# Kernel tuning notes

Measured on AMD Instinct MI355X. Metric: run time of the kernel, lower is better.

The kernel has to match this reference:

```python
import jax, jax.numpy as jnp
import numpy as np

NEG = -1e9  # masked_fill value


def _forward(input1, input2, wg1, wg2):
    S, E = input1.shape[0], wg1.shape[0]
    k = E // 4                      # expert_group_size
    num_2nd = E // 4
    capacity = int(2 * ((S + num_2nd - 1) // num_2nd))  # training-mode capacity, cf=1.0

    # --- first-level group gating ---
    group_logits = input1 @ wg1.T                     # [S,E]
    group_gates = jax.nn.softmax(group_logits.at[:, 0].set(NEG), axis=1)
    _, top_idx = jax.lax.top_k(group_gates, k)        # [S,k]
    rows = jnp.arange(S)[:, None]
    group_mask = jnp.zeros((S, E), dtype=bool).at[rows, top_idx].set(True)

    # --- second-level logits, masked to the selected group ---
    logits = input2 @ wg2.T                           # [S,E]
    gates = jax.nn.softmax(jnp.where(group_mask, logits, NEG), axis=1)

    # --- htop1gating ---
    indices1 = jnp.argmax(gates, axis=1)              # [S]
    mask1 = jax.nn.one_hot(indices1, E, dtype=jnp.int32)   # [S,E]
    gates1_s = (gates * mask1).sum(axis=1)            # [S]
    locations1 = jnp.cumsum(mask1, axis=0) - 1        # [S,E]

    me = jnp.mean(gates, axis=0)
    ce = jnp.mean(mask1.astype(gates.dtype), axis=0)
    l_aux = jnp.sum(me * ce) / num_2nd * (E * E)

    mask1 = mask1 * (locations1 < capacity).astype(mask1.dtype)
    locations1_s = jnp.sum(locations1 * mask1, axis=1)          # [S]
    gates1 = gates1_s[:, None] * mask1.astype(gates1_s.dtype)   # [S,E]
    locations1_sc = jax.nn.one_hot(locations1_s, capacity, dtype=gates1.dtype)  # [S,C]
    combine = gates1[:, :, None] * locations1_sc[:, None, :]    # [S,E,C]
    dispatch = combine.astype(bool)
    return l_aux, combine, dispatch


def setup_inputs() -> dict:
    key = jax.random.key(0)
    k1, k2, k3, k4 = jax.random.split(key, 4)
    S, D, E = 4096, 1024, 64
    return {
        "input1": jax.random.normal(k1, (S, D), dtype=jnp.float32),
        "input2": jax.random.normal(k2, (S, D), dtype=jnp.float32),
        "wg1": jax.random.normal(k3, (E, D), dtype=jnp.float32) * 0.02,
        "wg2": jax.random.normal(k4, (E, D), dtype=jnp.float32) * 0.02,
    }


def reference(input1, input2, wg1, wg2):
    return _forward(input1, input2, wg1, wg2)
```

## Files before the change

### kernel.cpp

```cpp
#include <hip/hip_runtime.h>
#include <cstdint>
#include <cstddef>

#define S_ROWS 4096
#define DIM 1024
#define NE 64
#define CAP 512
#define NEGV -1e9f

typedef float v4f __attribute__((ext_vector_type(4)));

__global__ __launch_bounds__(256) void zerofill(v4f* __restrict__ out4, long long n4,
                                                float* __restrict__ out, long long n) {
    long long i = (long long)blockIdx.x * blockDim.x + threadIdx.x;
    long long stride = (long long)gridDim.x * blockDim.x;
    v4f z = {0.f, 0.f, 0.f, 0.f};
    for (; i < n4; i += stride) __builtin_nontemporal_store(z, &out4[i]);
    if (blockIdx.x == 0 && threadIdx.x == 0) {
        for (long long j = n4 * 4; j < n; ++j) out[j] = 0.f;
    }
}

__global__ __launch_bounds__(256) void gemm64(const float* __restrict__ X1, const float* __restrict__ W1,
                                              const float* __restrict__ X2, const float* __restrict__ W2,
                                              float* __restrict__ L1, float* __restrict__ L2,
                                              float* __restrict__ Gg, int* __restrict__ Cg) {
    if (blockIdx.x == 0 && blockIdx.y == 0 && threadIdx.x < NE) {
        Gg[threadIdx.x] = 0.f;
        Cg[threadIdx.x] = 0;
    }
    const float* __restrict__ X = blockIdx.y ? X2 : X1;
    const float* __restrict__ W = blockIdx.y ? W2 : W1;
    float* __restrict__ L = blockIdx.y ? L2 : L1;

    __shared__ float As[32][68];
    __shared__ float Bs[64][68];

    const int tid = threadIdx.x;
    const int row0 = blockIdx.x * 32;
    const int tx = tid & 15;
    const int ty = tid >> 4;

    float acc[2][4] = {};

    for (int kk = 0; kk < DIM; kk += 64) {
        __syncthreads();
        #pragma unroll
        for (int p = 0; p < 2; ++p) {
            int r  = (tid >> 4) + p * 16;
            int c4 = (tid & 15) * 4;
            float4 a = *(const float4*)&X[(size_t)(row0 + r) * DIM + kk + c4];
            *(float4*)&As[r][c4] = a;
        }
        #pragma unroll
        for (int p = 0; p < 4; ++p) {
            int e  = (tid >> 4) + p * 16;
            int c4 = (tid & 15) * 4;
            float4 w = *(const float4*)&W[(size_t)e * DIM + kk + c4];
            Bs[c4 + 0][e] = w.x;
            Bs[c4 + 1][e] = w.y;
            Bs[c4 + 2][e] = w.z;
            Bs[c4 + 3][e] = w.w;
        }
        __syncthreads();
        #pragma unroll
        for (int k4 = 0; k4 < 64; k4 += 4) {
            float4 a[2], b[4];
            #pragma unroll
            for (int i = 0; i < 2; ++i) a[i] = *(float4*)&As[ty * 2 + i][k4];
            #pragma unroll
            for (int t = 0; t < 4; ++t) b[t] = *(float4*)&Bs[k4 + t][tx * 4];
            #pragma unroll
            for (int i = 0; i < 2; ++i) {
                acc[i][0] += a[i].x * b[0].x + a[i].y * b[1].x + a[i].z * b[2].x + a[i].w * b[3].x;
                acc[i][1] += a[i].x * b[0].y + a[i].y * b[1].y + a[i].z * b[2].y + a[i].w * b[3].y;
                acc[i][2] += a[i].x * b[0].z + a[i].y * b[1].z + a[i].z * b[2].z + a[i].w * b[3].z;
                acc[i][3] += a[i].x * b[0].w + a[i].y * b[1].w + a[i].z * b[2].w + a[i].w * b[3].w;
            }
        }
    }
    #pragma unroll
    for (int i = 0; i < 2; ++i) {
        float4 v; v.x = acc[i][0]; v.y = acc[i][1]; v.z = acc[i][2]; v.w = acc[i][3];
        *(float4*)&L[(size_t)(row0 + ty * 2 + i) * NE + tx * 4] = v;
    }
}

__global__ __launch_bounds__(256) void gatek2(const float* __restrict__ L1, const float* __restrict__ L2,
                                              int* __restrict__ eidx, float* __restrict__ gval,
                                              float* __restrict__ Gg, int* __restrict__ Cg) {
    __shared__ float sG[4][NE];
    __shared__ int hist[NE];
    const int wid = threadIdx.x >> 6, lane = threadIdx.x & 63;
    if (threadIdx.x < NE) hist[threadIdx.x] = 0;
    __syncthreads();

    const int r0 = blockIdx.x * 16 + wid * 4;
    float gacc = 0.f;
    #pragma unroll
    for (int i = 0; i < 4; ++i) {
        const int r = r0 + i;
        float l1 = L1[(size_t)r * NE + lane];
        if (lane == 0) l1 = NEGV;

        int cnt = 0;
        #pragma unroll
        for (int j = 0; j < 64; ++j) {
            float vj = __shfl(l1, j);
            cnt += (vj > l1 || (vj == l1 && j < lane));
        }
        const bool sel = cnt < 16;

        float l2 = L2[(size_t)r * NE + lane];
        float ml = sel ? l2 : NEGV;

        float m = ml;
        #pragma unroll
        for (int o = 32; o; o >>= 1) m = fmaxf(m, __shfl_xor(m, o));
        float ex = expf(ml - m);
        float sum = ex;
        #pragma unroll
        for (int o = 32; o; o >>= 1) sum += __shfl_xor(sum, o);
        float g = ex / sum;
        gacc += g;

        float bg = g; int bi = lane;
        #pragma unroll
        for (int o = 32; o; o >>= 1) {
            float og = __shfl_xor(bg, o);
            int   oi = __shfl_xor(bi, o);
            if (og > bg || (og == bg && oi < bi)) { bg = og; bi = oi; }
        }
        if (lane == 0) {
            eidx[r] = bi;
            gval[r] = bg;
            atomicAdd(&hist[bi], 1);
        }
    }
    sG[wid][lane] = gacc;
    __syncthreads();
    if (threadIdx.x < NE) {
        float g4 = sG[0][threadIdx.x] + sG[1][threadIdx.x] + sG[2][threadIdx.x] + sG[3][threadIdx.x];
        atomicAdd(&Gg[threadIdx.x], g4);
        atomicAdd(&Cg[threadIdx.x], hist[threadIdx.x]);
    }
}

__global__ void lauxfin(const float* __restrict__ Gg, const int* __restrict__ Cg,
                        float* __restrict__ out) {
    const int lane = threadIdx.x;
    float v = Gg[lane] * (float)Cg[lane];
    #pragma unroll
    for (int o = 32; o; o >>= 1) v += __shfl_xor(v, o);
    if (lane == 0) out[0] = v * (1.0f / 65536.0f);
}

__global__ __launch_bounds__(256) void scatterk(const int* __restrict__ eidx, const float* __restrict__ gval,
                                                float* __restrict__ out) {
    const int s = blockIdx.x;
    const int my = eidx[s];
    int cnt = 0;
    for (int j = threadIdx.x; j < s; j += 256) cnt += (eidx[j] == my);
    __shared__ int sc[4];
    #pragma unroll
    for (int o = 32; o; o >>= 1) cnt += __shfl_down(cnt, o);
    const int wid = threadIdx.x >> 6, lane = threadIdx.x & 63;
    if (lane == 0) sc[wid] = cnt;
    __syncthreads();
    if (threadIdx.x == 0) {
        int rank = sc[0] + sc[1] + sc[2] + sc[3];
        if (rank < CAP) {
            size_t base = 1 + (((size_t)s * NE + my) * CAP + (size_t)rank);
            out[base] = gval[s];
            out[base + (size_t)S_ROWS * NE * CAP] = 1.0f;
        }
    }
}

extern "C" void kernel_launch(void* const* d_in, const int* in_sizes, int n_in,
                              void* d_out, int out_size, void* d_ws, size_t ws_size,
                              hipStream_t stream) {
    const float* in1 = (const float*)d_in[0];
    const float* in2 = (const float*)d_in[1];
    const float* wg1 = (const float*)d_in[2];
    const float* wg2 = (const float*)d_in[3];
    float* out = (float*)d_out;

    float* L1   = (float*)d_ws;
    float* L2   = L1 + (size_t)S_ROWS * NE;
    int*   eidx = (int*)(L2 + (size_t)S_ROWS * NE);
    float* gv   = (float*)(eidx + S_ROWS);
    float* Gg   = gv + S_ROWS;
    int*   Cg   = (int*)(Gg + NE);

    long long n  = (long long)out_size;
    long long n4 = n >> 2;
    zerofill<<<4096, 256, 0, stream>>>((v4f*)out, n4, out, n);

    dim3 g(128, 2);
    gemm64<<<g, 256, 0, stream>>>(in1, wg1, in2, wg2, L1, L2, Gg, Cg);
    gatek2<<<S_ROWS / 16, 256, 0, stream>>>(L1, L2, eidx, gv, Gg, Cg);
    lauxfin<<<1, 64, 0, stream>>>(Gg, Cg, out);
    scatterk<<<S_ROWS, 256, 0, stream>>>(eidx, gv, out);
}
```

Before: 1.185 ms.

## Fuse zero-fill, both gate GEMMs and gating into one launch

Merges the output zero-fill, the two logit GEMMs and the gating step into one kernel. Extra blocks do the fill while the first 128 blocks compute both GEMMs into shared memory and gate directly from there. Global atomics for the aux loss are replaced by per-block slots, which a final kernel reduces together with the scatter. This removes launch gaps and the round trip of logits through global memory, and lets the gating compute overlap the bandwidth-bound fill. In exchange, the GEMM now runs on half as many blocks.

Result: faster. 1.075 ms (-9.2%).

```diff
diff --git a/kernel.cpp b/kernel.cpp
--- a/kernel.cpp
+++ b/kernel.cpp
@@ -7,100 +7,98 @@
 #define NE 64
 #define CAP 512
 #define NEGV -1e9f
+#define NGEMM 128
+#define NFILL 4096
 
 typedef float v4f __attribute__((ext_vector_type(4)));
 
-__global__ __launch_bounds__(256) void zerofill(v4f* __restrict__ out4, long long n4,
-                                                float* __restrict__ out, long long n) {
-    long long i = (long long)blockIdx.x * blockDim.x + threadIdx.x;
-    long long stride = (long long)gridDim.x * blockDim.x;
-    v4f z = {0.f, 0.f, 0.f, 0.f};
-    for (; i < n4; i += stride) __builtin_nontemporal_store(z, &out4[i]);
-    if (blockIdx.x == 0 && threadIdx.x == 0) {
-        for (long long j = n4 * 4; j < n; ++j) out[j] = 0.f;
-    }
-}
-
-__global__ __launch_bounds__(256) void gemm64(const float* __restrict__ X1, const float* __restrict__ W1,
+__global__ __launch_bounds__(256) void fusedA(const float* __restrict__ X1, const float* __restrict__ W1,
                                               const float* __restrict__ X2, const float* __restrict__ W2,
-                                              float* __restrict__ L1, float* __restrict__ L2,
-                                              float* __restrict__ Gg, int* __restrict__ Cg) {
-    if (blockIdx.x == 0 && blockIdx.y == 0 && threadIdx.x < NE) {
-        Gg[threadIdx.x] = 0.f;
-        Cg[threadIdx.x] = 0;
-    }
-    const float* __restrict__ X = blockIdx.y ? X2 : X1;
-    const float* __restrict__ W = blockIdx.y ? W2 : W1;
-    float* __restrict__ L = blockIdx.y ? L2 : L1;
+                                              int* __restrict__ eidx, float* __restrict__ gval,
+                                              float* __restrict__ Gslot, int* __restrict__ Cslot,
+                                              v4f* __restrict__ out4, long long n4,
+                                              float* __restrict__ out, long long n) {
+    const int bid = blockIdx.x;
+    const int tid = threadIdx.x;
 
     __shared__ float As[32][68];
     __shared__ float Bs[64][68];
-
-    const int tid = threadIdx.x;
-    const int row0 = blockIdx.x * 32;
+    __shared__ float Lg[2][32][68];
+    __shared__ float sG[4][NE];
+    __shared__ int   hist[NE];
+
+    if (bid >= NGEMM) {
+        long long i = (long long)(bid - NGEMM) * 256 + tid;
+        const long long stride = (long long)(gridDim.x - NGEMM) * 256;
+        v4f z = {0.f, 0.f, 0.f, 0.f};
+        for (; i < n4; i += stride) __builtin_nontemporal_store(z, &out4[i]);
+        if (bid == NGEMM && tid == 0)
+            for (long long j = n4 * 4; j < n; ++j) out[j] = 0.f;
+        return;
+    }
+
+    if (tid < NE) hist[tid] = 0;
+
+    const int row0 = bid * 32;
     const int tx = tid & 15;
     const int ty = tid >> 4;
 
-    float acc[2][4] = {};
-
-    for (int kk = 0; kk < DIM; kk += 64) {
-        __syncthreads();
-        #pragma unroll
-        for (int p = 0; p < 2; ++p) {
-            int r  = (tid >> 4) + p * 16;
-            int c4 = (tid & 15) * 4;
-            float4 a = *(const float4*)&X[(size_t)(row0 + r) * DIM + kk + c4];
-            *(float4*)&As[r][c4] = a;
-        }
-        #pragma unroll
-        for (int p = 0; p < 4; ++p) {
-            int e  = (tid >> 4) + p * 16;
-            int c4 = (tid & 15) * 4;
-            float4 w = *(const float4*)&W[(size_t)e * DIM + kk + c4];
-            Bs[c4 + 0][e] = w.x;
-            Bs[c4 + 1][e] = w.y;
-            Bs[c4 + 2][e] = w.z;
-            Bs[c4 + 3][e] = w.w;
-        }
-        __syncthreads();
-        #pragma unroll
-        for (int k4 = 0; k4 < 64; k4 += 4) {
-            float4 a[2], b[4];
-            #pragma unroll
-            for (int i = 0; i < 2; ++i) a[i] = *(float4*)&As[ty * 2 + i][k4];
-            #pragma unroll
-            for (int t = 0; t < 4; ++t) b[t] = *(float4*)&Bs[k4 + t][tx * 4];
-            #pragma unroll
-            for (int i = 0; i < 2; ++i) {
-                acc[i][0] += a[i].x * b[0].x + a[i].y * b[1].x + a[i].z * b[2].x + a[i].w * b[3].x;
-                acc[i][1] += a[i].x * b[0].y + a[i].y * b[1].y + a[i].z * b[2].y + a[i].w * b[3].y;
-                acc[i][2] += a[i].x * b[0].z + a[i].y * b[1].z + a[i].z * b[2].z + a[i].w * b[3].z;
-                acc[i][3] += a[i].x * b[0].w + a[i].y * b[1].w + a[i].z * b[2].w + a[i].w * b[3].w;
-            }
-        }
-    }
     #pragma unroll
-    for (int i = 0; i < 2; ++i) {
-        float4 v; v.x = acc[i][0]; v.y = acc[i][1]; v.z = acc[i][2]; v.w = acc[i][3];
-        *(float4*)&L[(size_t)(row0 + ty * 2 + i) * NE + tx * 4] = v;
-    }
-}
-
-__global__ __launch_bounds__(256) void gatek2(const float* __restrict__ L1, const float* __restrict__ L2,
-                                              int* __restrict__ eidx, float* __restrict__ gval,
-                                              float* __restrict__ Gg, int* __restrict__ Cg) {
-    __shared__ float sG[4][NE];
-    __shared__ int hist[NE];
-    const int wid = threadIdx.x >> 6, lane = threadIdx.x & 63;
-    if (threadIdx.x < NE) hist[threadIdx.x] = 0;
+    for (int m = 0; m < 2; ++m) {
+        const float* __restrict__ X = m ? X2 : X1;
+        const float* __restrict__ W = m ? W2 : W1;
+        float acc[2][4] = {};
+        for (int kk = 0; kk < DIM; kk += 64) {
+            __syncthreads();
+            #pragma unroll
+            for (int p = 0; p < 2; ++p) {
+                int r  = ty + p * 16;
+                int c4 = tx * 4;
+                float4 a = *(const float4*)&X[(size_t)(row0 + r) * DIM + kk + c4];
+                *(float4*)&As[r][c4] = a;
+            }
+            #pragma unroll
+            for (int p = 0; p < 4; ++p) {
+                int e  = ty + p * 16;
+                int c4 = tx * 4;
+                float4 w = *(const float4*)&W[(size_t)e * DIM + kk + c4];
+                Bs[c4 + 0][e] = w.x;
+                Bs[c4 + 1][e] = w.y;
+                Bs[c4 + 2][e] = w.z;
+                Bs[c4 + 3][e] = w.w;
+            }
+            __syncthreads();
+            #pragma unroll
+            for (int k4 = 0; k4 < 64; k4 += 4) {
+                float4 a[2], b[4];
+                #pragma unroll
+                for (int i = 0; i < 2; ++i) a[i] = *(float4*)&As[ty * 2 + i][k4];
+                #pragma unroll
+                for (int t = 0; t < 4; ++t) b[t] = *(float4*)&Bs[k4 + t][tx * 4];
+                #pragma unroll
+                for (int i = 0; i < 2; ++i) {
+                    acc[i][0] += a[i].x * b[0].x + a[i].y * b[1].x + a[i].z * b[2].x + a[i].w * b[3].x;
+                    acc[i][1] += a[i].x * b[0].y + a[i].y * b[1].y + a[i].z * b[2].y + a[i].w * b[3].y;
+                    acc[i][2] += a[i].x * b[0].z + a[i].y * b[1].z + a[i].z * b[2].z + a[i].w * b[3].z;
+                    acc[i][3] += a[i].x * b[0].w + a[i].y * b[1].w + a[i].z * b[2].w + a[i].w * b[3].w;
+                }
+            }
+        }
+        #pragma unroll
+        for (int i = 0; i < 2; ++i)
+            #pragma unroll
+            for (int t = 0; t < 4; ++t)
+                Lg[m][ty * 2 + i][tx * 4 + t] = acc[i][t];
+    }
     __syncthreads();
 
-    const int r0 = blockIdx.x * 16 + wid * 4;
+    const int wid = tid >> 6, lane = tid & 63;
     float gacc = 0.f;
     #pragma unroll
-    for (int i = 0; i < 4; ++i) {
-        const int r = r0 + i;
-        float l1 = L1[(size_t)r * NE + lane];
+    for (int i = 0; i < 8; ++i) {
+        const int lr = wid * 8 + i;
+        const int r  = row0 + lr;
+        float l1 = Lg[0][lr][lane];
         if (lane == 0) l1 = NEGV;
 
         int cnt = 0;
@@ -111,13 +109,13 @@
         }
         const bool sel = cnt < 16;
 
-        float l2 = L2[(size_t)r * NE + lane];
+        float l2 = Lg[1][lr][lane];
         float ml = sel ? l2 : NEGV;
 
-        float m = ml;
-        #pragma unroll
-        for (int o = 32; o; o >>= 1) m = fmaxf(m, __shfl_xor(m, o));
-        float ex = expf(ml - m);
+        float mx = ml;
+        #pragma unroll
+        for (int o = 32; o; o >>= 1) mx = fmaxf(mx, __shfl_xor(mx, o));
+        float ex = expf(ml - mx);
         float sum = ex;
         #pragma unroll
         for (int o = 32; o; o >>= 1) sum += __shfl_xor(sum, o);
@@ -139,25 +137,31 @@
     }
     sG[wid][lane] = gacc;
     __syncthreads();
-    if (threadIdx.x < NE) {
-        float g4 = sG[0][threadIdx.x] + sG[1][threadIdx.x] + sG[2][threadIdx.x] + sG[3][threadIdx.x];
-        atomicAdd(&Gg[threadIdx.x], g4);
-        atomicAdd(&Cg[threadIdx.x], hist[threadIdx.x]);
+    if (tid < NE) {
+        Gslot[bid * NE + tid] = sG[0][tid] + sG[1][tid] + sG[2][tid] + sG[3][tid];
+        Cslot[bid * NE + tid] = hist[tid];
     }
 }
 
-__global__ void lauxfin(const float* __restrict__ Gg, const int* __restrict__ Cg,
-                        float* __restrict__ out) {
-    const int lane = threadIdx.x;
-    float v = Gg[lane] * (float)Cg[lane];
-    #pragma unroll
-    for (int o = 32; o; o >>= 1) v += __shfl_xor(v, o);
-    if (lane == 0) out[0] = v * (1.0f / 65536.0f);
-}
-
-__global__ __launch_bounds__(256) void scatterk(const int* __restrict__ eidx, const float* __restrict__ gval,
-                                                float* __restrict__ out) {
+__global__ __launch_bounds__(256) void finishB(const int* __restrict__ eidx, const float* __restrict__ gval,
+                                               const float* __restrict__ Gslot, const int* __restrict__ Cslot,
+                                               float* __restrict__ out) {
     const int s = blockIdx.x;
+    if (s == S_ROWS) {
+        if (threadIdx.x < NE) {
+            const int e = threadIdx.x;
+            float Ge = 0.f; int Ce = 0;
+            for (int b = 0; b < NGEMM; ++b) {
+                Ge += Gslot[b * NE + e];
+                Ce += Cslot[b * NE + e];
+            }
+            float v = Ge * (float)Ce;
+            #pragma unroll
+            for (int o = 32; o; o >>= 1) v += __shfl_xor(v, o);
+            if (e == 0) out[0] = v * (1.0f / 65536.0f);
+        }
+        return;
+    }
     const int my = eidx[s];
     int cnt = 0;
     for (int j = threadIdx.x; j < s; j += 256) cnt += (eidx[j] == my);
@@ -186,20 +190,16 @@
     const float* wg2 = (const float*)d_in[3];
     float* out = (float*)d_out;
 
-    float* L1   = (float*)d_ws;
-    float* L2   = L1 + (size_t)S_ROWS * NE;
-    int*   eidx = (int*)(L2 + (size_t)S_ROWS * NE);
-    float* gv   = (float*)(eidx + S_ROWS);
-    float* Gg   = gv + S_ROWS;
-    int*   Cg   = (int*)(Gg + NE);
+    int*   eidx  = (int*)d_ws;
+    float* gv    = (float*)(eidx + S_ROWS);
+    float* Gslot = gv + S_ROWS;
+    int*   Cslot = (int*)(Gslot + NGEMM * NE);
 
     long long n  = (long long)out_size;
     long long n4 = n >> 2;
-    zerofill<<<4096, 256, 0, stream>>>((v4f*)out, n4, out, n);
-
-    dim3 g(128, 2);
-    gemm64<<<g, 256, 0, stream>>>(in1, wg1, in2, wg2, L1, L2, Gg, Cg);
-    gatek2<<<S_ROWS / 16, 256, 0, stream>>>(L1, L2, eidx, gv, Gg, Cg);
-    lauxfin<<<1, 64, 0, stream>>>(Gg, Cg, out);
-    scatterk<<<S_ROWS, 256, 0, stream>>>(eidx, gv, out);
+
+    fusedA<<<NGEMM + NFILL, 256, 0, stream>>>(in1, wg1, in2, wg2,
+                                              eidx, gv, Gslot, Cslot,
+                                              (v4f*)out, n4, out, n);
+    finishB<<<S_ROWS + 1, 256, 0, stream>>>(eidx, gv, Gslot, Cslot, out);
 }
```
